# Kernel tuning notes

Measured on AMD Instinct MI355X. Metric: run time of the kernel, lower is better.

## Reference

```python
import jax, jax.numpy as jnp
import numpy as np

LORA_ALPHA = 32.0
LORA_R = 16
SCALING = LORA_ALPHA / LORA_R


def setup_inputs() -> dict:
    key = jax.random.key(0)
    k1, k2, k3, k4, k5, k6 = jax.random.split(key, 6)
    B, S, D_IN, D_OUT = 4, 2048, 4096, 4096
    x = jax.random.normal(k1, (B, S, D_IN), dtype=jnp.float32)
    # int8 weight stored as int8 (spec uses int32 range [-127,127])
    qweight = jax.random.randint(k2, (D_OUT, D_IN), -127, 128, dtype=jnp.int32).astype(jnp.int8)
    # per-output-channel dequant scales (bf16 in torch; fp32 here for reference fidelity)
    scales = jax.random.uniform(k3, (D_OUT,), dtype=jnp.float32, minval=0.5, maxval=1.5) * 0.01
    bias = jax.random.normal(k4, (D_OUT,), dtype=jnp.float32) * 0.02
    # kaiming-uniform-like init for lora_A, zeros for lora_B would kill the LoRA
    # branch; use small random lora_B so the add path is exercised.
    bound = 1.0 / np.sqrt(D_IN)
    lora_A = jax.random.uniform(k5, (LORA_R, D_IN), dtype=jnp.float32, minval=-bound, maxval=bound)
    lora_B = jax.random.normal(k6, (D_OUT, LORA_R), dtype=jnp.float32) * 0.01
    return {"x": x, "qweight": qweight, "scales": scales, "bias": bias,
            "lora_A": lora_A, "lora_B": lora_B}


def reference(x, qweight, scales, bias, lora_A, lora_B):
    # W8A16 dequant: per-output-channel scale on int8 weight [out, in]
    w = qweight.astype(x.dtype) * scales[:, None]           # [out, in]
    base = jnp.einsum('bsi,oi->bso', x, w) + bias           # F.linear(x, W, b)
    # LoRA low-rank correction: (x @ A^T) @ B^T * scaling
    lora = jnp.einsum('bsr,or->bso', jnp.einsum('bsi,ri->bsr', x, lora_A), lora_B)
    return base + lora * SCALING
```

## Files before the change

### kernel.cpp

```cpp
#include <hip/hip_runtime.h>

#define LORA_RANK 16
#define SCALING 2.0f

using bf16x8 = __attribute__((ext_vector_type(8))) __bf16;
using bf16x4 = __attribute__((ext_vector_type(4))) __bf16;
using f32x4  = __attribute__((ext_vector_type(4))) float;
using i32x4  = __attribute__((ext_vector_type(4))) int;

#define GLB(p) ((const __attribute__((address_space(1))) void*)(p))
#define LDS(p) ((__attribute__((address_space(3))) void*)(p))

__global__ __launch_bounds__(256) void lora_mat_kernel(
    const float* __restrict__ lA, const float* __restrict__ lB,
    __bf16* __restrict__ L, int N, int K)
{
    const int i0 = blockIdx.x * 256;
    const int o0 = blockIdx.y * 64;
    const int t  = threadIdx.x;

    __shared__ float As[LORA_RANK][256];
    __shared__ float Bs[64][LORA_RANK];

    #pragma unroll
    for (int j = 0; j < 16; ++j) {
        int idx = t + j * 256;
        int r = idx >> 8, c = idx & 255;
        As[r][c] = lA[(long)r * K + i0 + c];
    }
    #pragma unroll
    for (int j = 0; j < 4; ++j) {
        int idx = t + j * 256;
        int o = idx >> 4, r = idx & 15;
        Bs[o][r] = lB[(long)(o0 + o) * LORA_RANK + r] * SCALING;
    }
    __syncthreads();

    const int ol = t & 63;
    const int iq = t >> 6;
    const int o  = o0 + ol;

    float bb[LORA_RANK];
    #pragma unroll
    for (int r = 0; r < LORA_RANK; ++r) bb[r] = Bs[ol][r];

    __bf16* lrow = L + (long)o * K + i0 + iq * 64;
    #pragma unroll
    for (int c = 0; c < 16; ++c) {
        const int ib = iq * 64 + c * 4;
        f32x4 v = {0.f, 0.f, 0.f, 0.f};
        #pragma unroll
        for (int r = 0; r < LORA_RANK; ++r) {
            v[0] += bb[r] * As[r][ib + 0];
            v[1] += bb[r] * As[r][ib + 1];
            v[2] += bb[r] * As[r][ib + 2];
            v[3] += bb[r] * As[r][ib + 3];
        }
        bf16x4 wv;
        wv[0] = (__bf16)v[0]; wv[1] = (__bf16)v[1];
        wv[2] = (__bf16)v[2]; wv[3] = (__bf16)v[3];
        *(bf16x4*)(lrow + c * 4) = wv;
    }
}

__global__ __launch_bounds__(256) void quant_w_kernel(
    const int* __restrict__ q, const float* __restrict__ scales,
    const __bf16* __restrict__ L, signed char* __restrict__ W8,
    float* __restrict__ sn, int K)
{
    const int o = blockIdx.x, t = threadIdx.x;
    __shared__ float buf[4096];
    __shared__ float red[256];

    const int4*   qr = (const int4*)(q + (long)o * K);
    const bf16x4* Lr = (const bf16x4*)(L + (long)o * K);
    const float   s  = scales[o];

    float mx = 0.f;
    #pragma unroll
    for (int j = 0; j < 4; ++j) {
        int c = t + j * 256;
        int4   qv = qr[c];
        bf16x4 lv = Lr[c];
        f32x4 w;
        w[0] = (float)qv.x * s + (float)lv[0];
        w[1] = (float)qv.y * s + (float)lv[1];
        w[2] = (float)qv.z * s + (float)lv[2];
        w[3] = (float)qv.w * s + (float)lv[3];
        *(f32x4*)&buf[c * 4] = w;
        mx = fmaxf(mx, fmaxf(fmaxf(fabsf(w[0]), fabsf(w[1])),
                             fmaxf(fabsf(w[2]), fabsf(w[3]))));
    }
    red[t] = mx;
    __syncthreads();
    for (int s2 = 128; s2 > 0; s2 >>= 1) {
        if (t < s2) red[t] = fmaxf(red[t], red[t + s2]);
        __syncthreads();
    }
    const float gmax = fmaxf(red[0], 1e-30f);
    const float winv = 127.0f / gmax;

    int* wrow = (int*)(W8 + (long)o * K);
    #pragma unroll
    for (int j = 0; j < 4; ++j) {
        int c = t + j * 256;
        f32x4 w = *(const f32x4*)&buf[c * 4];
        int c0 = (int)rintf(fminf(fmaxf(w[0] * winv, -127.f), 127.f));
        int c1 = (int)rintf(fminf(fmaxf(w[1] * winv, -127.f), 127.f));
        int c2 = (int)rintf(fminf(fmaxf(w[2] * winv, -127.f), 127.f));
        int c3 = (int)rintf(fminf(fmaxf(w[3] * winv, -127.f), 127.f));
        wrow[c] = (c0 & 255) | ((c1 & 255) << 8) | ((c2 & 255) << 16) | (c3 << 24);
    }
    if (t == 0) sn[o] = gmax / 127.0f;
}

__global__ __launch_bounds__(256) void quant_x_kernel(
    const float* __restrict__ X, signed char* __restrict__ X8,
    float* __restrict__ sxm, int K)
{
    const int m = blockIdx.x, t = threadIdx.x;
    __shared__ float red[256];

    const f32x4* xr = (const f32x4*)(X + (long)m * K);
    f32x4 v[4];
    float mx = 0.f;
    #pragma unroll
    for (int j = 0; j < 4; ++j) {
        v[j] = xr[t + j * 256];
        mx = fmaxf(mx, fmaxf(fmaxf(fabsf(v[j][0]), fabsf(v[j][1])),
                             fmaxf(fabsf(v[j][2]), fabsf(v[j][3]))));
    }
    red[t] = mx;
    __syncthreads();
    for (int s2 = 128; s2 > 0; s2 >>= 1) {
        if (t < s2) red[t] = fmaxf(red[t], red[t + s2]);
        __syncthreads();
    }
    const float gmax = fmaxf(red[0], 1e-30f);
    const float xinv = 127.0f / gmax;

    int* xrow = (int*)(X8 + (long)m * K);
    #pragma unroll
    for (int j = 0; j < 4; ++j) {
        int c0 = (int)rintf(fminf(fmaxf(v[j][0] * xinv, -127.f), 127.f));
        int c1 = (int)rintf(fminf(fmaxf(v[j][1] * xinv, -127.f), 127.f));
        int c2 = (int)rintf(fminf(fmaxf(v[j][2] * xinv, -127.f), 127.f));
        int c3 = (int)rintf(fminf(fmaxf(v[j][3] * xinv, -127.f), 127.f));
        xrow[t + j * 256] = (c0 & 255) | ((c1 & 255) << 8) | ((c2 & 255) << 16) | (c3 << 24);
    }
    if (t == 0) sxm[m] = gmax / 127.0f;
}

#define VMW0  asm volatile("s_waitcnt vmcnt(0)" ::: "memory")
#define SB0   __builtin_amdgcn_sched_barrier(0)

#define RD4(base, off) (*(const i32x4*)((base) + (off)))

#define MFI(mi, nj, A, B) \
    acc[mi][nj] = __builtin_amdgcn_mfma_i32_16x16x64_i8(A, B, acc[mi][nj], 0, 0, 0)

#define STAGE_I8(dA, dB) do { \
    __builtin_amdgcn_global_load_lds(GLB(pB),          LDS((dB) + wb),         16, 0, 0); \
    __builtin_amdgcn_global_load_lds(GLB(pB + rk),     LDS((dB) + wb +  8192), 16, 0, 0); \
    __builtin_amdgcn_global_load_lds(GLB(pB + 2 * rk), LDS((dB) + wb + 16384), 16, 0, 0); \
    __builtin_amdgcn_global_load_lds(GLB(pB + 3 * rk), LDS((dB) + wb + 24576), 16, 0, 0); \
    __builtin_amdgcn_global_load_lds(GLB(pA),          LDS((dA) + wb),         16, 0, 0); \
    __builtin_amdgcn_global_load_lds(GLB(pA + rk),     LDS((dA) + wb +  8192), 16, 0, 0); \
    __builtin_amdgcn_global_load_lds(GLB(pA + 2 * rk), LDS((dA) + wb + 16384), 16, 0, 0); \
    __builtin_amdgcn_global_load_lds(GLB(pA + 3 * rk), LDS((dA) + wb + 24576), 16, 0, 0); } while (0)

#define ADVP8(a) do { pA += (a); pB += (a); } while (0)

#define TILE_I8(Ac, Bc, DOSTAGE) do { \
    const char* _ac = (Ac); const char* _bc = (Bc); \
    DOSTAGE; \
    {  \
      i32x4 b0 = RD4(_bc, bRow +    0 + kc0); \
      i32x4 b1 = RD4(_bc, bRow + 2048 + kc0); \
      i32x4 b2 = RD4(_bc, bRow + 4096 + kc0); \
      i32x4 b3 = RD4(_bc, bRow + 6144 + kc0); \
      i32x4 a0 = RD4(_ac, aRow +     0 + kc0); \
      i32x4 a1 = RD4(_ac, aRow +  2048 + kc0); \
      i32x4 a2 = RD4(_ac, aRow +  4096 + kc0); \
      i32x4 a3 = RD4(_ac, aRow +  6144 + kc0); \
      i32x4 a4 = RD4(_ac, aRow +  8192 + kc0); \
      i32x4 a5 = RD4(_ac, aRow + 10240 + kc0); \
      i32x4 a6 = RD4(_ac, aRow + 12288 + kc0); \
      i32x4 a7 = RD4(_ac, aRow + 14336 + kc0); \
      __builtin_amdgcn_s_setprio(1); \
      MFI(0,0,a0,b0); MFI(1,0,a1,b0); MFI(2,0,a2,b0); MFI(3,0,a3,b0); \
      MFI(4,0,a4,b0); MFI(5,0,a5,b0); MFI(6,0,a6,b0); MFI(7,0,a7,b0); \
      MFI(0,1,a0,b1); MFI(1,1,a1,b1); MFI(2,1,a2,b1); MFI(3,1,a3,b1); \
      MFI(4,1,a4,b1); MFI(5,1,a5,b1); MFI(6,1,a6,b1); MFI(7,1,a7,b1); \
      MFI(0,2,a0,b2); MFI(1,2,a1,b2); MFI(2,2,a2,b2); MFI(3,2,a3,b2); \
      MFI(4,2,a4,b2); MFI(5,2,a5,b2); MFI(6,2,a6,b2); MFI(7,2,a7,b2); \
      MFI(0,3,a0,b3); MFI(1,3,a1,b3); MFI(2,3,a2,b3); MFI(3,3,a3,b3); \
      MFI(4,3,a4,b3); MFI(5,3,a5,b3); MFI(6,3,a6,b3); MFI(7,3,a7,b3); \
      __builtin_amdgcn_s_setprio(0); \
    } \
    {  \
      i32x4 b0 = RD4(_bc, bRow +    0 + kc1); \
      i32x4 b1 = RD4(_bc, bRow + 2048 + kc1); \
      i32x4 b2 = RD4(_bc, bRow + 4096 + kc1); \
      i32x4 b3 = RD4(_bc, bRow + 6144 + kc1); \
      i32x4 a0 = RD4(_ac, aRow +     0 + kc1); \
      i32x4 a1 = RD4(_ac, aRow +  2048 + kc1); \
      i32x4 a2 = RD4(_ac, aRow +  4096 + kc1); \
      i32x4 a3 = RD4(_ac, aRow +  6144 + kc1); \
      i32x4 a4 = RD4(_ac, aRow +  8192 + kc1); \
      i32x4 a5 = RD4(_ac, aRow + 10240 + kc1); \
      i32x4 a6 = RD4(_ac, aRow + 12288 + kc1); \
      i32x4 a7 = RD4(_ac, aRow + 14336 + kc1); \
      __builtin_amdgcn_s_setprio(1); \
      MFI(0,0,a0,b0); MFI(1,0,a1,b0); MFI(2,0,a2,b0); MFI(3,0,a3,b0); \
      MFI(4,0,a4,b0); MFI(5,0,a5,b0); MFI(6,0,a6,b0); MFI(7,0,a7,b0); \
      MFI(0,1,a0,b1); MFI(1,1,a1,b1); MFI(2,1,a2,b1); MFI(3,1,a3,b1); \
      MFI(4,1,a4,b1); MFI(5,1,a5,b1); MFI(6,1,a6,b1); MFI(7,1,a7,b1); \
      MFI(0,2,a0,b2); MFI(1,2,a1,b2); MFI(2,2,a2,b2); MFI(3,2,a3,b2); \
      MFI(4,2,a4,b2); MFI(5,2,a5,b2); MFI(6,2,a6,b2); MFI(7,2,a7,b2); \
      MFI(0,3,a0,b3); MFI(1,3,a1,b3); MFI(2,3,a2,b3); MFI(3,3,a3,b3); \
      MFI(4,3,a4,b3); MFI(5,3,a5,b3); MFI(6,3,a6,b3); MFI(7,3,a7,b3); \
      __builtin_amdgcn_s_setprio(0); \
    } \
    VMW0; \
    __builtin_amdgcn_s_barrier(); \
    SB0; \
  } while (0)

__global__ __launch_bounds__(512, 2) void gemm_i8_kernel(
    const signed char* __restrict__ X8, const signed char* __restrict__ W8,
    const float* __restrict__ sxm, const float* __restrict__ sn,
    const float* __restrict__ bias, float* __restrict__ C,
    int M, int N, int K)
{
    __shared__ __align__(16) char smem[131072];

    const int t = threadIdx.x, wid = t >> 6, lane = t & 63;
    const int wr = wid >> 2, wc = wid & 3;
    const int l15 = lane & 15, l7 = lane & 7, lk = lane >> 4;

    const int nwg = gridDim.x;
    int bid = blockIdx.x;
    if ((nwg & 7) == 0) bid = (bid & 7) * (nwg >> 3) + (bid >> 3);
    const int ntn = N >> 8;
    const int m0 = (bid / ntn) << 8, n0 = (bid % ntn) << 8;

    const int sr = t >> 3;
    const int ch = (t & 7) ^ (sr & 7);
    const long rk = 64L * K;
    const signed char* pA = X8 + (long)(m0 + sr) * K + ch * 16;
    const signed char* pB = W8 + (long)(n0 + sr) * K + ch * 16;

    const int wb = wid * 1024;

    const int aRow = (wr * 128 + l15) * 128;
    const int bRow = (wc * 64  + l15) * 128;
    const int kc0  = ((lk    ) ^ l7) << 4;
    const int kc1  = ((lk + 4) ^ l7) << 4;

    char* const bA0 = smem;
    char* const bB0 = smem + 32768;
    char* const bA1 = smem + 65536;
    char* const bB1 = smem + 98304;

    i32x4 acc[8][4] = {};

    const int nkt = K >> 7;

    STAGE_I8(bA0, bB0);
    ADVP8(nkt > 1 ? 128 : 0);
    VMW0;
    __builtin_amdgcn_s_barrier();
    SB0;

    for (int kt = 0; kt < nkt; kt += 2) {
        const long adv1 = (kt + 2 < nkt) ? 128 : 0;
        const long adv2 = (kt + 3 < nkt) ? 128 : 0;
        TILE_I8(bA0, bB0, { STAGE_I8(bA1, bB1); ADVP8(adv1); });
        TILE_I8(bA1, bB1, { STAGE_I8(bA0, bB0); ADVP8(adv2); });
    }

    #pragma unroll
    for (int nj = 0; nj < 4; ++nj) {
        const int col = n0 + wc * 64 + nj * 16 + l15;
        const float scol = sn[col];
        const float bv   = bias[col];
        #pragma unroll
        for (int mi = 0; mi < 8; ++mi) {
            const long rowb = (long)m0 + wr * 128 + mi * 16 + (lane >> 4) * 4;
            const f32x4 sx4 = *(const f32x4*)(sxm + rowb);
            float* Cp = C + rowb * N + col;
            Cp[0]       = (float)acc[mi][nj][0] * (sx4[0] * scol) + bv;
            Cp[(long)N] = (float)acc[mi][nj][1] * (sx4[1] * scol) + bv;
            Cp[2L * N]  = (float)acc[mi][nj][2] * (sx4[2] * scol) + bv;
            Cp[3L * N]  = (float)acc[mi][nj][3] * (sx4[3] * scol) + bv;
        }
    }
}

__global__ __launch_bounds__(256) void fold_weight_kernel(
    const int* __restrict__ q, const float* __restrict__ scales,
    const float* __restrict__ lA, const float* __restrict__ lB,
    __bf16* __restrict__ W, int N, int K)
{
    const int i0 = blockIdx.x * 256;
    const int o0 = blockIdx.y * 64;
    const int t  = threadIdx.x;

    __shared__ float As[LORA_RANK][256];
    __shared__ float Bs[64][LORA_RANK];

    #pragma unroll
    for (int j = 0; j < 16; ++j) {
        int idx = t + j * 256;
        As[idx >> 8][idx & 255] = lA[(long)(idx >> 8) * K + i0 + (idx & 255)];
    }
    #pragma unroll
    for (int j = 0; j < 4; ++j) {
        int idx = t + j * 256;
        Bs[idx >> 4][idx & 15] = lB[(long)(o0 + (idx >> 4)) * LORA_RANK + (idx & 15)] * SCALING;
    }
    __syncthreads();

    const int ol = t & 63, iq = t >> 6, o = o0 + ol;
    const float sc = scales[o];
    float bb[LORA_RANK];
    #pragma unroll
    for (int r = 0; r < LORA_RANK; ++r) bb[r] = Bs[ol][r];

    const int* qrow = q + (long)o * K + i0 + iq * 64;
    __bf16*    wrow = W + (long)o * K + i0 + iq * 64;
    #pragma unroll
    for (int c = 0; c < 16; ++c) {
        int4 q4 = *(const int4*)(qrow + c * 4);
        float v[4] = {(float)q4.x * sc, (float)q4.y * sc, (float)q4.z * sc, (float)q4.w * sc};
        const int ib = iq * 64 + c * 4;
        #pragma unroll
        for (int r = 0; r < LORA_RANK; ++r) {
            v[0] += bb[r] * As[r][ib + 0]; v[1] += bb[r] * As[r][ib + 1];
            v[2] += bb[r] * As[r][ib + 2]; v[3] += bb[r] * As[r][ib + 3];
        }
        bf16x4 wv; wv[0] = (__bf16)v[0]; wv[1] = (__bf16)v[1];
        wv[2] = (__bf16)v[2]; wv[3] = (__bf16)v[3];
        *(bf16x4*)(wrow + c * 4) = wv;
    }
}

__global__ __launch_bounds__(256) void cvt_x_kernel(
    const float* __restrict__ X, __bf16* __restrict__ Xb, long n)
{
    const long stride = (long)gridDim.x * 256 * 8;
    for (long i = ((long)blockIdx.x * 256 + threadIdx.x) * 8; i < n; i += stride) {
        f32x4 a = *(const f32x4*)(X + i);
        f32x4 b = *(const f32x4*)(X + i + 4);
        bf16x8 v;
        #pragma unroll
        for (int j = 0; j < 4; ++j) { v[j] = (__bf16)a[j]; v[j + 4] = (__bf16)b[j]; }
        *(bf16x8*)(Xb + i) = v;
    }
}

#define RD8(base, off) (*(const bf16x8*)((base) + (off)))
#define MF(mi, nj, A, B) \
    acc[mi][nj] = __builtin_amdgcn_mfma_f32_16x16x32_bf16(A, B, acc[mi][nj], 0, 0, 0)
#define SWEEP16(qb, A0, A1, A2, A3, B0, B1, B2, B3) \
    MF((qb)+0,0,A0,B0); MF((qb)+1,0,A1,B0); MF((qb)+2,0,A2,B0); MF((qb)+3,0,A3,B0); \
    MF((qb)+0,1,A0,B1); MF((qb)+1,1,A1,B1); MF((qb)+2,1,A2,B1); MF((qb)+3,1,A3,B1); \
    MF((qb)+0,2,A0,B2); MF((qb)+1,2,A1,B2); MF((qb)+2,2,A2,B2); MF((qb)+3,2,A3,B2); \
    MF((qb)+0,3,A0,B3); MF((qb)+1,3,A1,B3); MF((qb)+2,3,A2,B3); MF((qb)+3,3,A3,B3);
#define STAGE_ALL(dA, dB) do { \
    __builtin_amdgcn_global_load_lds(GLB(pB0),  LDS((dB) + wb),         16, 0, 0); \
    __builtin_amdgcn_global_load_lds(GLB(pB0b), LDS((dB) + wb +  8192), 16, 0, 0); \
    __builtin_amdgcn_global_load_lds(GLB(pB1),  LDS((dB) + wb + 16384), 16, 0, 0); \
    __builtin_amdgcn_global_load_lds(GLB(pB1b), LDS((dB) + wb + 24576), 16, 0, 0); \
    __builtin_amdgcn_global_load_lds(GLB(pA0),  LDS((dA) + wb),         16, 0, 0); \
    __builtin_amdgcn_global_load_lds(GLB(pA0b), LDS((dA) + wb +  8192), 16, 0, 0); \
    __builtin_amdgcn_global_load_lds(GLB(pA1),  LDS((dA) + wb + 16384), 16, 0, 0); \
    __builtin_amdgcn_global_load_lds(GLB(pA1b), LDS((dA) + wb + 24576), 16, 0, 0); } while (0)
#define ADVP(a) do { pA0 += (a); pA0b += (a); pA1 += (a); pA1b += (a); \
                     pB0 += (a); pB0b += (a); pB1 += (a); pB1b += (a); } while (0)
#define TILE3(Ac, Bc, DOSTAGE) do { \
    const char* _ac = (Ac); const char* _bc = (Bc); \
    DOSTAGE; \
    { bf16x8 b0 = RD8(_bc, bRow +    0 + kc0); bf16x8 b1 = RD8(_bc, bRow + 2048 + kc0); \
      bf16x8 b2 = RD8(_bc, bRow + 4096 + kc0); bf16x8 b3 = RD8(_bc, bRow + 6144 + kc0); \
      bf16x8 a0 = RD8(_ac, aRow +     0 + kc0); bf16x8 a1 = RD8(_ac, aRow +  2048 + kc0); \
      bf16x8 a2 = RD8(_ac, aRow +  4096 + kc0); bf16x8 a3 = RD8(_ac, aRow +  6144 + kc0); \
      bf16x8 a4 = RD8(_ac, aRow +  8192 + kc0); bf16x8 a5 = RD8(_ac, aRow + 10240 + kc0); \
      bf16x8 a6 = RD8(_ac, aRow + 12288 + kc0); bf16x8 a7 = RD8(_ac, aRow + 14336 + kc0); \
      __builtin_amdgcn_s_setprio(1); \
      SWEEP16(0, a0, a1, a2, a3, b0, b1, b2, b3); \
      SWEEP16(4, a4, a5, a6, a7, b0, b1, b2, b3); \
      __builtin_amdgcn_s_setprio(0); } \
    { bf16x8 b0 = RD8(_bc, bRow +    0 + kc1); bf16x8 b1 = RD8(_bc, bRow + 2048 + kc1); \
      bf16x8 b2 = RD8(_bc, bRow + 4096 + kc1); bf16x8 b3 = RD8(_bc, bRow + 6144 + kc1); \
      bf16x8 a0 = RD8(_ac, aRow +     0 + kc1); bf16x8 a1 = RD8(_ac, aRow +  2048 + kc1); \
      bf16x8 a2 = RD8(_ac, aRow +  4096 + kc1); bf16x8 a3 = RD8(_ac, aRow +  6144 + kc1); \
      bf16x8 a4 = RD8(_ac, aRow +  8192 + kc1); bf16x8 a5 = RD8(_ac, aRow + 10240 + kc1); \
      bf16x8 a6 = RD8(_ac, aRow + 12288 + kc1); bf16x8 a7 = RD8(_ac, aRow + 14336 + kc1); \
      __builtin_amdgcn_s_setprio(1); \
      SWEEP16(0, a0, a1, a2, a3, b0, b1, b2, b3); \
      SWEEP16(4, a4, a5, a6, a7, b0, b1, b2, b3); \
      __builtin_amdgcn_s_setprio(0); } \
    VMW0; \
    __builtin_amdgcn_s_barrier(); \
    SB0; \
  } while (0)

__global__ __launch_bounds__(512, 2) void gemm256_kernel(
    const __bf16* __restrict__ Xb, const __bf16* __restrict__ W,
    const float* __restrict__ bias, float* __restrict__ C,
    int M, int N, int K)
{
    __shared__ __align__(16) char smem[131072];

    const int t = threadIdx.x, wid = t >> 6, lane = t & 63;
    const int wr = wid >> 2, wc = wid & 3;
    const int l15 = lane & 15, l7 = lane & 7, lk = lane >> 4;

    const int nwg = gridDim.x;
    int bid = blockIdx.x;
    if ((nwg & 7) == 0) bid = (bid & 7) * (nwg >> 3) + (bid >> 3);
    const int ntn = N >> 8;
    const int m0 = (bid / ntn) << 8, n0 = (bid % ntn) << 8;

    const int sr = t >> 3;
    const int sc = (t & 7) ^ (sr & 7);
    const __bf16* pA0  = Xb + (long)(m0 +       sr) * K + sc * 8;
    const __bf16* pA0b = Xb + (long)(m0 +  64 + sr) * K + sc * 8;
    const __bf16* pA1  = Xb + (long)(m0 + 128 + sr) * K + sc * 8;
    const __bf16* pA1b = Xb + (long)(m0 + 192 + sr) * K + sc * 8;
    const __bf16* pB0  = W  + (long)(n0 +       sr) * K + sc * 8;
    const __bf16* pB0b = W  + (long)(n0 +  64 + sr) * K + sc * 8;
    const __bf16* pB1  = W  + (long)(n0 + 128 + sr) * K + sc * 8;
    const __bf16* pB1b = W  + (long)(n0 + 192 + sr) * K + sc * 8;

    const int wb = wid * 1024;
    const int aRow = (wr * 128 + l15) * 128;
    const int bRow = (wc * 64  + l15) * 128;
    const int kc0  = ((lk    ) ^ l7) << 4;
    const int kc1  = ((lk + 4) ^ l7) << 4;

    char* const bA0 = smem;
    char* const bB0 = smem + 32768;
    char* const bA1 = smem + 65536;
    char* const bB1 = smem + 98304;

    f32x4 acc[8][4] = {};
    const int nkt = K >> 6;

    STAGE_ALL(bA0, bB0);
    ADVP(nkt > 1 ? 64 : 0);
    VMW0;
    __builtin_amdgcn_s_barrier();
    SB0;

    for (int kt = 0; kt < nkt; kt += 2) {
        const long adv1 = (kt + 2 < nkt) ? 64 : 0;
        const long adv2 = (kt + 3 < nkt) ? 64 : 0;
        TILE3(bA0, bB0, { STAGE_ALL(bA1, bB1); ADVP(adv1); });
        TILE3(bA1, bB1, { STAGE_ALL(bA0, bB0); ADVP(adv2); });
    }

    #pragma unroll
    for (int nj = 0; nj < 4; ++nj) {
        const int col = n0 + wc * 64 + nj * 16 + l15;
        const float bv = bias[col];
        #pragma unroll
        for (int mi = 0; mi < 8; ++mi) {
            const long row = (long)m0 + wr * 128 + mi * 16 + (lane >> 4) * 4;
            float* Cp = C + row * N + col;
            Cp[0]       = acc[mi][nj][0] + bv;
            Cp[(long)N] = acc[mi][nj][1] + bv;
            Cp[2L * N]  = acc[mi][nj][2] + bv;
            Cp[3L * N]  = acc[mi][nj][3] + bv;
        }
    }
}

__global__ __launch_bounds__(256) void fallback_gemm(
    const float* __restrict__ X, const int* __restrict__ q,
    const float* __restrict__ scales, const float* __restrict__ bias,
    const float* __restrict__ lA, const float* __restrict__ lB,
    float* __restrict__ C, int M, int N, int K)
{
    __shared__ float Xs[64][17];
    __shared__ float Ws[64][17];
    __shared__ float At[LORA_RANK][16];
    __shared__ float Bt[64][LORA_RANK];

    const int ntn = N >> 6;
    const int m0 = (blockIdx.x / ntn) << 6, n0 = (blockIdx.x % ntn) << 6;
    const int t = threadIdx.x;

    for (int j = t; j < 64 * LORA_RANK; j += 256)
        Bt[j >> 4][j & 15] = lB[(long)(n0 + (j >> 4)) * LORA_RANK + (j & 15)] * SCALING;

    const int tr = (t & 15) * 4, tc = (t >> 4) * 4;
    float acc[4][4] = {};

    for (int k0 = 0; k0 < K; k0 += 16) {
        __syncthreads();
        for (int j = t; j < 1024; j += 256)
            Xs[j >> 4][j & 15] = X[(long)(m0 + (j >> 4)) * K + k0 + (j & 15)];
        At[t >> 4][t & 15] = lA[(long)(t >> 4) * K + k0 + (t & 15)];
        __syncthreads();
        for (int j = t; j < 1024; j += 256) {
            int o = j >> 4, kk = j & 15;
            float v = (float)q[(long)(n0 + o) * K + k0 + kk] * scales[n0 + o];
            #pragma unroll
            for (int r = 0; r < LORA_RANK; ++r) v += Bt[o][r] * At[r][kk];
            Ws[o][kk] = v;
        }
        __syncthreads();
        #pragma unroll 4
        for (int kk = 0; kk < 16; ++kk)
            #pragma unroll
            for (int i = 0; i < 4; ++i)
                #pragma unroll
                for (int j = 0; j < 4; ++j)
                    acc[i][j] += Xs[tr + i][kk] * Ws[tc + j][kk];
    }
    __syncthreads();
    #pragma unroll
    for (int i = 0; i < 4; ++i)
        #pragma unroll
        for (int j = 0; j < 4; ++j)
            C[(long)(m0 + tr + i) * N + n0 + tc + j] = acc[i][j] + bias[n0 + tc + j];
}

extern "C" void kernel_launch(void* const* d_in, const int* in_sizes, int n_in,
                              void* d_out, int out_size, void* d_ws, size_t ws_size,
                              hipStream_t stream)
{
    const float* x      = (const float*)d_in[0];
    const int*   qw     = (const int*)d_in[1];
    const float* scales = (const float*)d_in[2];
    const float* bias   = (const float*)d_in[3];
    const float* lA     = (const float*)d_in[4];
    const float* lB     = (const float*)d_in[5];
    float*       out    = (float*)d_out;

    const int K = in_sizes[4] / LORA_RANK;
    const int N = in_sizes[2];
    const int M = in_sizes[0] / K;

    const size_t i8need = (size_t)N * K + (size_t)M * K + (size_t)(M + N) * 4
                        + (size_t)N * K * 2 + 256;
    const bool i8_ok = (K == 4096) && (M % 256) == 0 && (N % 256) == 0 &&
                       ws_size >= i8need;
    const size_t wbytes = (size_t)N * K * sizeof(__bf16);
    const size_t xbytes = (size_t)M * K * sizeof(__bf16);
    const bool big_ok = (M % 256) == 0 && (N % 256) == 0 && (K % 256) == 0 &&
                        ((K >> 6) % 2) == 0 && ws_size >= wbytes + xbytes;

    if (i8_ok) {
        signed char* W8  = (signed char*)d_ws;
        signed char* X8  = W8 + (size_t)N * K;
        float*       sxm = (float*)(X8 + (size_t)M * K);
        float*       sn  = sxm + M;
        __bf16*      L   = (__bf16*)(sn + N);

        dim3 g1(K / 256, N / 64);
        lora_mat_kernel<<<g1, 256, 0, stream>>>(lA, lB, L, N, K);
        quant_w_kernel<<<N, 256, 0, stream>>>(qw, scales, L, W8, sn, K);
        quant_x_kernel<<<M, 256, 0, stream>>>(x, X8, sxm, K);
        const int nwg = (M / 256) * (N / 256);
        gemm_i8_kernel<<<nwg, 512, 0, stream>>>(X8, W8, sxm, sn, bias, out, M, N, K);
    } else if (big_ok) {
        __bf16* W  = (__bf16*)d_ws;
        __bf16* Xb = (__bf16*)((char*)d_ws + wbytes);
        dim3 g1(K / 256, N / 64);
        fold_weight_kernel<<<g1, 256, 0, stream>>>(qw, scales, lA, lB, W, N, K);
        cvt_x_kernel<<<2048, 256, 0, stream>>>(x, Xb, (long)M * K);
        const int nwg = (M / 256) * (N / 256);
        gemm256_kernel<<<nwg, 512, 0, stream>>>(Xb, W, bias, out, M, N, K);
    } else {
        fallback_gemm<<<(M / 64) * (N / 64), 256, 0, stream>>>(
            x, qw, scales, bias, lA, lB, out, M, N, K);
    }
}
```

Before: 220.0 us.

## Shrink int8 GEMM tile to 256x128 and software-pipeline LDS fragment reads

```diff
diff --git a/kernel.cpp b/kernel.cpp
--- a/kernel.cpp
+++ b/kernel.cpp
@@ -152,80 +152,43 @@
 }
 
 #define VMW0  asm volatile("s_waitcnt vmcnt(0)" ::: "memory")
-#define SB0   __builtin_amdgcn_sched_barrier(0)
+#define VMW6  asm volatile("s_waitcnt vmcnt(6)" ::: "memory")
+#define LGKM0 asm volatile("s_waitcnt lgkmcnt(0)" ::: "memory")
 
 #define RD4(base, off) (*(const i32x4*)((base) + (off)))
 
 #define MFI(mi, nj, A, B) \
     acc[mi][nj] = __builtin_amdgcn_mfma_i32_16x16x64_i8(A, B, acc[mi][nj], 0, 0, 0)
 
-#define STAGE_I8(dA, dB) do { \
-    __builtin_amdgcn_global_load_lds(GLB(pB),          LDS((dB) + wb),         16, 0, 0); \
-    __builtin_amdgcn_global_load_lds(GLB(pB + rk),     LDS((dB) + wb +  8192), 16, 0, 0); \
-    __builtin_amdgcn_global_load_lds(GLB(pB + 2 * rk), LDS((dB) + wb + 16384), 16, 0, 0); \
-    __builtin_amdgcn_global_load_lds(GLB(pB + 3 * rk), LDS((dB) + wb + 24576), 16, 0, 0); \
+#define DECLF(p) i32x4 p##a0, p##a1, p##a2, p##a3, p##b0, p##b1, p##b2, p##b3
+
+#define READF(p, ac, bc, kc) do { \
+    p##b0 = RD4(bc, bRow +    0 + (kc)); \
+    p##b1 = RD4(bc, bRow + 2048 + (kc)); \
+    p##b2 = RD4(bc, bRow + 4096 + (kc)); \
+    p##b3 = RD4(bc, bRow + 6144 + (kc)); \
+    p##a0 = RD4(ac, aRow +    0 + (kc)); \
+    p##a1 = RD4(ac, aRow + 2048 + (kc)); \
+    p##a2 = RD4(ac, aRow + 4096 + (kc)); \
+    p##a3 = RD4(ac, aRow + 6144 + (kc)); } while (0)
+
+#define MFMAS(p) do { \
+    __builtin_amdgcn_s_setprio(1); \
+    MFI(0,0,p##a0,p##b0); MFI(1,0,p##a1,p##b0); MFI(2,0,p##a2,p##b0); MFI(3,0,p##a3,p##b0); \
+    MFI(0,1,p##a0,p##b1); MFI(1,1,p##a1,p##b1); MFI(2,1,p##a2,p##b1); MFI(3,1,p##a3,p##b1); \
+    MFI(0,2,p##a0,p##b2); MFI(1,2,p##a1,p##b2); MFI(2,2,p##a2,p##b2); MFI(3,2,p##a3,p##b2); \
+    MFI(0,3,p##a0,p##b3); MFI(1,3,p##a1,p##b3); MFI(2,3,p##a2,p##b3); MFI(3,3,p##a3,p##b3); \
+    __builtin_amdgcn_s_setprio(0); } while (0)
+
+#define STAGE6(dA, dB) do { \
     __builtin_amdgcn_global_load_lds(GLB(pA),          LDS((dA) + wb),         16, 0, 0); \
     __builtin_amdgcn_global_load_lds(GLB(pA + rk),     LDS((dA) + wb +  8192), 16, 0, 0); \
     __builtin_amdgcn_global_load_lds(GLB(pA + 2 * rk), LDS((dA) + wb + 16384), 16, 0, 0); \
-    __builtin_amdgcn_global_load_lds(GLB(pA + 3 * rk), LDS((dA) + wb + 24576), 16, 0, 0); } while (0)
+    __builtin_amdgcn_global_load_lds(GLB(pA + 3 * rk), LDS((dA) + wb + 24576), 16, 0, 0); \
+    __builtin_amdgcn_global_load_lds(GLB(pB),          LDS((dB) + wb),         16, 0, 0); \
+    __builtin_amdgcn_global_load_lds(GLB(pB + rk),     LDS((dB) + wb +  8192), 16, 0, 0); } while (0)
 
 #define ADVP8(a) do { pA += (a); pB += (a); } while (0)
-
-#define TILE_I8(Ac, Bc, DOSTAGE) do { \
-    const char* _ac = (Ac); const char* _bc = (Bc); \
-    DOSTAGE; \
-    {  \
-      i32x4 b0 = RD4(_bc, bRow +    0 + kc0); \
-      i32x4 b1 = RD4(_bc, bRow + 2048 + kc0); \
-      i32x4 b2 = RD4(_bc, bRow + 4096 + kc0); \
-      i32x4 b3 = RD4(_bc, bRow + 6144 + kc0); \
-      i32x4 a0 = RD4(_ac, aRow +     0 + kc0); \
-      i32x4 a1 = RD4(_ac, aRow +  2048 + kc0); \
-      i32x4 a2 = RD4(_ac, aRow +  4096 + kc0); \
-      i32x4 a3 = RD4(_ac, aRow +  6144 + kc0); \
-      i32x4 a4 = RD4(_ac, aRow +  8192 + kc0); \
-      i32x4 a5 = RD4(_ac, aRow + 10240 + kc0); \
-      i32x4 a6 = RD4(_ac, aRow + 12288 + kc0); \
-      i32x4 a7 = RD4(_ac, aRow + 14336 + kc0); \
-      __builtin_amdgcn_s_setprio(1); \
-      MFI(0,0,a0,b0); MFI(1,0,a1,b0); MFI(2,0,a2,b0); MFI(3,0,a3,b0); \
-      MFI(4,0,a4,b0); MFI(5,0,a5,b0); MFI(6,0,a6,b0); MFI(7,0,a7,b0); \
-      MFI(0,1,a0,b1); MFI(1,1,a1,b1); MFI(2,1,a2,b1); MFI(3,1,a3,b1); \
-      MFI(4,1,a4,b1); MFI(5,1,a5,b1); MFI(6,1,a6,b1); MFI(7,1,a7,b1); \
-      MFI(0,2,a0,b2); MFI(1,2,a1,b2); MFI(2,2,a2,b2); MFI(3,2,a3,b2); \
-      MFI(4,2,a4,b2); MFI(5,2,a5,b2); MFI(6,2,a6,b2); MFI(7,2,a7,b2); \
-      MFI(0,3,a0,b3); MFI(1,3,a1,b3); MFI(2,3,a2,b3); MFI(3,3,a3,b3); \
-      MFI(4,3,a4,b3); MFI(5,3,a5,b3); MFI(6,3,a6,b3); MFI(7,3,a7,b3); \
-      __builtin_amdgcn_s_setprio(0); \
-    } \
-    {  \
-      i32x4 b0 = RD4(_bc, bRow +    0 + kc1); \
-      i32x4 b1 = RD4(_bc, bRow + 2048 + kc1); \
-      i32x4 b2 = RD4(_bc, bRow + 4096 + kc1); \
-      i32x4 b3 = RD4(_bc, bRow + 6144 + kc1); \
-      i32x4 a0 = RD4(_ac, aRow +     0 + kc1); \
-      i32x4 a1 = RD4(_ac, aRow +  2048 + kc1); \
-      i32x4 a2 = RD4(_ac, aRow +  4096 + kc1); \
-      i32x4 a3 = RD4(_ac, aRow +  6144 + kc1); \
-      i32x4 a4 = RD4(_ac, aRow +  8192 + kc1); \
-      i32x4 a5 = RD4(_ac, aRow + 10240 + kc1); \
-      i32x4 a6 = RD4(_ac, aRow + 12288 + kc1); \
-      i32x4 a7 = RD4(_ac, aRow + 14336 + kc1); \
-      __builtin_amdgcn_s_setprio(1); \
-      MFI(0,0,a0,b0); MFI(1,0,a1,b0); MFI(2,0,a2,b0); MFI(3,0,a3,b0); \
-      MFI(4,0,a4,b0); MFI(5,0,a5,b0); MFI(6,0,a6,b0); MFI(7,0,a7,b0); \
-      MFI(0,1,a0,b1); MFI(1,1,a1,b1); MFI(2,1,a2,b1); MFI(3,1,a3,b1); \
-      MFI(4,1,a4,b1); MFI(5,1,a5,b1); MFI(6,1,a6,b1); MFI(7,1,a7,b1); \
-      MFI(0,2,a0,b2); MFI(1,2,a1,b2); MFI(2,2,a2,b2); MFI(3,2,a3,b2); \
-      MFI(4,2,a4,b2); MFI(5,2,a5,b2); MFI(6,2,a6,b2); MFI(7,2,a7,b2); \
-      MFI(0,3,a0,b3); MFI(1,3,a1,b3); MFI(2,3,a2,b3); MFI(3,3,a3,b3); \
-      MFI(4,3,a4,b3); MFI(5,3,a5,b3); MFI(6,3,a6,b3); MFI(7,3,a7,b3); \
-      __builtin_amdgcn_s_setprio(0); \
-    } \
-    VMW0; \
-    __builtin_amdgcn_s_barrier(); \
-    SB0; \
-  } while (0)
 
 __global__ __launch_bounds__(512, 2) void gemm_i8_kernel(
     const signed char* __restrict__ X8, const signed char* __restrict__ W8,
@@ -233,17 +196,17 @@
     const float* __restrict__ bias, float* __restrict__ C,
     int M, int N, int K)
 {
-    __shared__ __align__(16) char smem[131072];
+    __shared__ __align__(16) char smem[98304];
 
     const int t = threadIdx.x, wid = t >> 6, lane = t & 63;
-    const int wr = wid >> 2, wc = wid & 3;
+    const int wr = wid >> 1, wc = wid & 1;
     const int l15 = lane & 15, l7 = lane & 7, lk = lane >> 4;
 
     const int nwg = gridDim.x;
     int bid = blockIdx.x;
     if ((nwg & 7) == 0) bid = (bid & 7) * (nwg >> 3) + (bid >> 3);
-    const int ntn = N >> 8;
-    const int m0 = (bid / ntn) << 8, n0 = (bid % ntn) << 8;
+    const int ntn = N >> 7;
+    const int m0 = (bid / ntn) << 8, n0 = (bid % ntn) << 7;
 
     const int sr = t >> 3;
     const int ch = (t & 7) ^ (sr & 7);
@@ -253,31 +216,48 @@
 
     const int wb = wid * 1024;
 
-    const int aRow = (wr * 128 + l15) * 128;
-    const int bRow = (wc * 64  + l15) * 128;
+    const int aRow = (wr * 64 + l15) * 128;
+    const int bRow = (wc * 64 + l15) * 128;
     const int kc0  = ((lk    ) ^ l7) << 4;
     const int kc1  = ((lk + 4) ^ l7) << 4;
 
     char* const bA0 = smem;
     char* const bB0 = smem + 32768;
-    char* const bA1 = smem + 65536;
-    char* const bB1 = smem + 98304;
-
-    i32x4 acc[8][4] = {};
+    char* const bA1 = smem + 49152;
+    char* const bB1 = smem + 81920;
+
+    i32x4 acc[4][4] = {};
 
     const int nkt = K >> 7;
 
-    STAGE_I8(bA0, bB0);
+    STAGE6(bA0, bB0);
     ADVP8(nkt > 1 ? 128 : 0);
-    VMW0;
+    STAGE6(bA1, bB1);
+    ADVP8(nkt > 2 ? 128 : 0);
+    VMW6;
     __builtin_amdgcn_s_barrier();
-    SB0;
+
+    DECLF(x);
+    DECLF(y);
+    READF(x, bA0, bB0, kc0);
 
     for (int kt = 0; kt < nkt; kt += 2) {
-        const long adv1 = (kt + 2 < nkt) ? 128 : 0;
-        const long adv2 = (kt + 3 < nkt) ? 128 : 0;
-        TILE_I8(bA0, bB0, { STAGE_I8(bA1, bB1); ADVP8(adv1); });
-        TILE_I8(bA1, bB1, { STAGE_I8(bA0, bB0); ADVP8(adv2); });
+        READF(y, bA0, bB0, kc1);
+        MFMAS(x);
+        LGKM0; VMW0;
+        __builtin_amdgcn_s_barrier();
+        STAGE6(bA0, bB0);
+        ADVP8((kt + 3 < nkt) ? 128 : 0);
+        READF(x, bA1, bB1, kc0);
+        MFMAS(y);
+        READF(y, bA1, bB1, kc1);
+        MFMAS(x);
+        LGKM0; VMW0;
+        __builtin_amdgcn_s_barrier();
+        STAGE6(bA1, bB1);
+        ADVP8((kt + 4 < nkt) ? 128 : 0);
+        READF(x, bA0, bB0, kc0);
+        MFMAS(y);
     }
 
     #pragma unroll
@@ -286,8 +266,8 @@
         const float scol = sn[col];
         const float bv   = bias[col];
         #pragma unroll
-        for (int mi = 0; mi < 8; ++mi) {
-            const long rowb = (long)m0 + wr * 128 + mi * 16 + (lane >> 4) * 4;
+        for (int mi = 0; mi < 4; ++mi) {
+            const long rowb = (long)m0 + wr * 64 + mi * 16 + (lane >> 4) * 4;
             const f32x4 sx4 = *(const f32x4*)(sxm + rowb);
             float* Cp = C + rowb * N + col;
             Cp[0]       = (float)acc[mi][nj][0] * (sx4[0] * scol) + bv;
@@ -404,7 +384,6 @@
       __builtin_amdgcn_s_setprio(0); } \
     VMW0; \
     __builtin_amdgcn_s_barrier(); \
-    SB0; \
   } while (0)
 
 __global__ __launch_bounds__(512, 2) void gemm256_kernel(
@@ -453,7 +432,6 @@
     ADVP(nkt > 1 ? 64 : 0);
     VMW0;
     __builtin_amdgcn_s_barrier();
-    SB0;
 
     for (int kt = 0; kt < nkt; kt += 2) {
         const long adv1 = (kt + 2 < nkt) ? 64 : 0;
@@ -547,7 +525,7 @@
 
     const size_t i8need = (size_t)N * K + (size_t)M * K + (size_t)(M + N) * 4
                         + (size_t)N * K * 2 + 256;
-    const bool i8_ok = (K == 4096) && (M % 256) == 0 && (N % 256) == 0 &&
+    const bool i8_ok = (K == 4096) && (M % 256) == 0 && (N % 128) == 0 &&
                        ws_size >= i8need;
     const size_t wbytes = (size_t)N * K * sizeof(__bf16);
     const size_t xbytes = (size_t)M * K * sizeof(__bf16);
@@ -565,7 +543,7 @@
         lora_mat_kernel<<<g1, 256, 0, stream>>>(lA, lB, L, N, K);
         quant_w_kernel<<<N, 256, 0, stream>>>(qw, scales, L, W8, sn, K);
         quant_x_kernel<<<M, 256, 0, stream>>>(x, X8, sxm, K);
-        const int nwg = (M / 256) * (N / 256);
+        const int nwg = (M / 256) * (N / 128);
         gemm_i8_kernel<<<nwg, 512, 0, stream>>>(X8, W8, sxm, sn, bias, out, M, N, K);
     } else if (big_ok) {
         __bf16* W  = (__bf16*)d_ws;
```

Result: slower. 229.0 us (+4.1%).
